# Kernel optimization log

Hardware: AMD Instinct MI355X
Metric: run time of the kernel (lower is better)

The kernel has to match this reference:

```python
import jax, jax.numpy as jnp
import numpy as np

NUM_SELECTS = 2
NOISE_EPS = 0.01
LOSS_COEF = 0.01
INV_SQRT2 = 0.7071067811865476


def _phi(z):
    # standard normal CDF
    return 0.5 * (1.0 + jax.lax.erf(z * INV_SQRT2))


def _cv_squared(v, eps=1e-10):
    # torch .var() uses unbiased estimator (ddof=1)
    return jnp.var(v, ddof=1) / (jnp.mean(v) ** 2 + eps)


def setup_inputs() -> dict:
    key = jax.random.key(0)
    ks = jax.random.split(key, 5)
    T, D, E = 8192, 4096, 16
    return {
        "x": jax.random.normal(ks[0], (T, D), jnp.float32),
        "gate_w1": jax.random.normal(ks[1], (E, D), jnp.float32) * 0.02,
        "gate_w2": jax.random.normal(ks[2], (E, E), jnp.float32) * 0.02,
        "noise_w": jax.random.normal(ks[3], (E, D), jnp.float32) * 0.02,
        "noise": jax.random.normal(ks[4], (T, E), jnp.float32),
    }


def reference(x, gate_w1, gate_w2, noise_w, noise):
    T = x.shape[0]
    # gate network: Linear -> tanh -> Linear (no biases)
    logits_gate = jnp.tanh(x @ gate_w1.T) @ gate_w2.T          # [T, E]
    noise_control = jax.nn.softplus(x @ noise_w.T) + NOISE_EPS  # [T, E]
    logits_noise = noise * noise_control                        # [T, E]
    logits = logits_gate + logits_noise

    # top (k+1) for load-balancing thresholds
    top_logits, top_indices = jax.lax.top_k(logits, NUM_SELECTS + 1)
    top_k_logits = top_logits[:, :NUM_SELECTS]
    top_k_indices = top_indices[:, :NUM_SELECTS]
    top_k_scores = jax.nn.softmax(top_k_logits, axis=1)

    # importance: scatter top-k scores back to [T, E]
    rows = jnp.arange(T)[:, None]
    scores_filtered = jnp.zeros_like(logits).at[rows, top_k_indices].set(top_k_scores)
    importance = scores_filtered.sum(0)  # [E]

    # load: prob each expert would be in the top-k under the noise model
    thr_in = top_logits[:, NUM_SELECTS][:, None]        # (k+1)-th largest
    thr_out = top_logits[:, NUM_SELECTS - 1][:, None]   # k-th largest
    is_in = logits_noise > thr_in
    prob_if_in = _phi((logits_gate - thr_in) / noise_control)
    prob_if_out = _phi((logits_gate - thr_out) / noise_control)
    load = jnp.where(is_in, prob_if_in, prob_if_out).sum(0)  # [E]

    gate_loss = (_cv_squared(importance) + _cv_squared(load)) * LOSS_COEF
    return top_k_indices, top_k_scores, gate_loss
```

## Files before the change

### kernel.cpp

```cpp
#include <hip/hip_runtime.h>
#include <math.h>

#define TT 8192
#define DD 4096

typedef float  f32x4  __attribute__((ext_vector_type(4)));
typedef short  bf16x8 __attribute__((ext_vector_type(8)));
typedef unsigned int u32;

typedef __attribute__((address_space(3))) void        lds_vp;
typedef const __attribute__((address_space(1))) void  gbl_vp;
#define GLD(gp_, lp_) __builtin_amdgcn_global_load_lds((gbl_vp*)(gp_), (lds_vp*)(lp_), 16, 0, 0)

__global__ __launch_bounds__(128)
void split_w(const float* __restrict__ gw1, const float* __restrict__ nw,
             u32* __restrict__ wfrag) {
  const int s = blockIdx.x;
  const int t = threadIdx.x;
  const int h = t >> 6, l = t & 63;
  const int e = h * 16 + (l & 15);
  const float* src = ((e < 16) ? (gw1 + (size_t)e * DD) : (nw + (size_t)(e - 16) * DD))
                     + s * 32 + ((l >> 4) << 3);
  float f[8];
  *(float4*)&f[0] = *(const float4*)src;
  *(float4*)&f[4] = *(const float4*)(src + 4);
  u32 u0[8], u1[8], u2[8];
#pragma unroll
  for (int i = 0; i < 8; ++i) {
    u0[i] = __float_as_uint(f[i]);
    const float r1 = f[i] - __uint_as_float(u0[i] & 0xFFFF0000u);
    u1[i] = __float_as_uint(r1);
    const float r2 = r1 - __uint_as_float(u1[i] & 0xFFFF0000u);
    u2[i] = __float_as_uint(r2);
  }
  const size_t base = ((size_t)s * 2 + h) * 256 + l * 4;
#define PK(U) make_uint4((U[0]>>16)|(U[1]&0xFFFF0000u), (U[2]>>16)|(U[3]&0xFFFF0000u), \
                         (U[4]>>16)|(U[5]&0xFFFF0000u), (U[6]>>16)|(U[7]&0xFFFF0000u))
  *(uint4*)(wfrag + base)                 = PK(u0);
  *(uint4*)(wfrag + base + 128 * 512)     = PK(u1);
  *(uint4*)(wfrag + base + 2 * 128 * 512) = PK(u2);
#undef PK
}

__global__ __launch_bounds__(1024, 4)
void gate_mega(const float* __restrict__ x, const u32* __restrict__ wfrag,
               const float* __restrict__ noise, const float* __restrict__ gw2,
               float* __restrict__ out, float* __restrict__ part2) {
  __shared__ __align__(16) u32 ldsb[2][8][6][256];
  __shared__ float red[8][1024];
  __shared__ float sg2[256];
  const int t = threadIdx.x;
  const int v = t >> 6, l = t & 63;
  const int w = v & 7;
  const int m = v >> 3;
  const int rt = blockIdx.x;
  if (t < 256) sg2[t] = gw2[t];

  const int r = l & 15, c = l >> 4;
  const float* xp = x + (size_t)(rt * 32 + m * 16 + r) * DD + w * 512 + (c << 3);

  const u32* srcb[3];
  u32* dst0[3];
  u32* dst1[3];
#pragma unroll
  for (int i = 0; i < 3; ++i) {
    const int q = 3 * v + i, s = q / 6, p = q % 6;
    srcb[i] = wfrag + (size_t)(p >> 1) * 65536 + (p & 1) * 256
                    + (size_t)s * 16 * 512 + (l << 2);
    dst0[i] = &ldsb[0][s][p][0];
    dst1[i] = &ldsb[1][s][p][0];
  }

#pragma unroll
  for (int i = 0; i < 3; ++i) GLD(srcb[i], dst0[i]);
  asm volatile("s_waitcnt vmcnt(0)" ::: "memory");
  asm volatile("s_barrier" ::: "memory");

  f32x4 ag0 = {0,0,0,0}, ag1 = ag0, ag2 = ag0, an0 = ag0, an1 = ag0, an2 = ag0;

#pragma unroll 2
  for (int sl = 0; sl < 16; ++sl) {
    if (sl + 1 < 16) {
#pragma unroll
      for (int i = 0; i < 3; ++i)
        GLD(srcb[i] + (size_t)(sl + 1) * 512, (sl & 1) ? dst0[i] : dst1[i]);
    }

    const u32* wb = &ldsb[sl & 1][w][0][0] + (l << 2);
    const bf16x8 bg0 = *(const bf16x8*)(wb);
    const bf16x8 bn0 = *(const bf16x8*)(wb + 256);
    const bf16x8 bg1 = *(const bf16x8*)(wb + 512);
    const bf16x8 bn1 = *(const bf16x8*)(wb + 768);
    const bf16x8 bg2 = *(const bf16x8*)(wb + 1024);
    const bf16x8 bn2 = *(const bf16x8*)(wb + 1280);

    float f[8];
    *(float4*)&f[0] = *(const float4*)(xp + sl * 32);
    *(float4*)&f[4] = *(const float4*)(xp + sl * 32 + 4);

    u32 pk[12] __attribute__((aligned(16)));
#pragma unroll
    for (int p = 0; p < 4; ++p) {
      const float fa = f[2 * p], fb = f[2 * p + 1];
      const u32  a  = __float_as_uint(fa);
      const float ra1 = fa - __uint_as_float(a & 0xFFFF0000u);
      const u32  a1 = __float_as_uint(ra1);
      const float ra2 = ra1 - __uint_as_float(a1 & 0xFFFF0000u);
      const u32  a2 = __float_as_uint(ra2);
      const u32  b  = __float_as_uint(fb);
      const float rb1 = fb - __uint_as_float(b & 0xFFFF0000u);
      const u32  b1 = __float_as_uint(rb1);
      const float rb2 = rb1 - __uint_as_float(b1 & 0xFFFF0000u);
      const u32  b2 = __float_as_uint(rb2);
      pk[p]     = (a  >> 16) | (b  & 0xFFFF0000u);
      pk[4 + p] = (a1 >> 16) | (b1 & 0xFFFF0000u);
      pk[8 + p] = (a2 >> 16) | (b2 & 0xFFFF0000u);
    }
    const bf16x8 a0 = *(const bf16x8*)&pk[0];
    const bf16x8 a1 = *(const bf16x8*)&pk[4];
    const bf16x8 a2 = *(const bf16x8*)&pk[8];

    ag0 = __builtin_amdgcn_mfma_f32_16x16x32_bf16(a0, bg0, ag0, 0, 0, 0);
    an0 = __builtin_amdgcn_mfma_f32_16x16x32_bf16(a0, bn0, an0, 0, 0, 0);
    ag1 = __builtin_amdgcn_mfma_f32_16x16x32_bf16(a0, bg1, ag1, 0, 0, 0);
    an1 = __builtin_amdgcn_mfma_f32_16x16x32_bf16(a0, bn1, an1, 0, 0, 0);
    ag2 = __builtin_amdgcn_mfma_f32_16x16x32_bf16(a1, bg0, ag2, 0, 0, 0);
    an2 = __builtin_amdgcn_mfma_f32_16x16x32_bf16(a1, bn0, an2, 0, 0, 0);
    ag0 = __builtin_amdgcn_mfma_f32_16x16x32_bf16(a0, bg2, ag0, 0, 0, 0);
    an0 = __builtin_amdgcn_mfma_f32_16x16x32_bf16(a0, bn2, an0, 0, 0, 0);
    ag1 = __builtin_amdgcn_mfma_f32_16x16x32_bf16(a1, bg1, ag1, 0, 0, 0);
    an1 = __builtin_amdgcn_mfma_f32_16x16x32_bf16(a1, bn1, an1, 0, 0, 0);
    ag2 = __builtin_amdgcn_mfma_f32_16x16x32_bf16(a2, bg0, ag2, 0, 0, 0);
    an2 = __builtin_amdgcn_mfma_f32_16x16x32_bf16(a2, bn0, an2, 0, 0, 0);

    asm volatile("s_waitcnt vmcnt(0)" ::: "memory");
    asm volatile("s_barrier" ::: "memory");
  }

  const f32x4 cg = ag0 + ag1 + ag2;
  const f32x4 cn = an0 + an1 + an2;
#pragma unroll
  for (int j = 0; j < 4; ++j) {
    red[w][m * 512 + r * 16 + (c * 4 + j)]        = cg[j];
    red[w][m * 512 + (16 + r) * 16 + (c * 4 + j)] = cn[j];
  }
  __syncthreads();
  {
    float s = red[0][t];
#pragma unroll
    for (int ww = 1; ww < 8; ++ww) s += red[ww][t];
    red[0][t] = s;
  }
  __syncthreads();

  if (t < 32) {
    const int mg = t >> 4, rr = t & 15;
    const int row = rt * 32 + t;
    float dot[32];
#pragma unroll
    for (int e = 0; e < 32; ++e) dot[e] = red[0][mg * 512 + e * 16 + rr];
    float h[16];
#pragma unroll
    for (int e = 0; e < 16; ++e) h[e] = tanhf(dot[e]);
    float lg[16], nc[16], ln[16], lo[16];
#pragma unroll
    for (int j = 0; j < 16; ++j) {
      float s = 0.f;
#pragma unroll
      for (int e = 0; e < 16; ++e) s = fmaf(h[e], sg2[j * 16 + e], s);
      lg[j] = s;
      const float vv = dot[16 + j];
      nc[j] = fmaxf(vv, 0.f) + log1pf(expf(-fabsf(vv))) + 0.01f;
      ln[j] = noise[(size_t)row * 16 + j] * nc[j];
      lo[j] = lg[j] + ln[j];
    }
    int i0 = 0; float m0 = lo[0];
#pragma unroll
    for (int j = 1; j < 16; ++j) if (lo[j] > m0) { m0 = lo[j]; i0 = j; }
    int i1 = -1; float m1 = -1e30f;
#pragma unroll
    for (int j = 0; j < 16; ++j) if (j != i0 && lo[j] > m1) { m1 = lo[j]; i1 = j; }
    float m2 = -1e30f;
#pragma unroll
    for (int j = 0; j < 16; ++j) if (j != i0 && j != i1 && lo[j] > m2) m2 = lo[j];

    const float e1 = expf(m1 - m0);
    const float s0 = 1.f / (1.f + e1);
    const float s1 = e1 / (1.f + e1);
    out[(size_t)row * 2]             = (float)i0;
    out[(size_t)row * 2 + 1]         = (float)i1;
    out[16384 + (size_t)row * 2]     = s0;
    out[16384 + (size_t)row * 2 + 1] = s1;

    float cacc[32];
#pragma unroll
    for (int j = 0; j < 16; ++j) {
      cacc[j] = (j == i0) ? s0 : ((j == i1) ? s1 : 0.f);
      const bool in = ln[j] > m2;
      const float thr = in ? m2 : m1;
      const float z = (lg[j] - thr) / nc[j];
      cacc[16 + j] = 0.5f * (1.f + erff(z * 0.70710678118654752f));
    }
#pragma unroll
    for (int off = 1; off < 16; off <<= 1) {
#pragma unroll
      for (int k = 0; k < 32; ++k) cacc[k] += __shfl_xor(cacc[k], off, 16);
    }
    const int g = rt * 2 + mg;
    float v0 = 0.f, v1 = 0.f;
#pragma unroll
    for (int k = 0; k < 16; ++k) if (rr == k) { v0 = cacc[k]; v1 = cacc[16 + k]; }
    part2[(size_t)g * 32 + rr]      = v0;
    part2[(size_t)g * 32 + 16 + rr] = v1;
  }
}

__global__ __launch_bounds__(256)
void gate_loss_k(const float* __restrict__ part2, float* __restrict__ out) {
  __shared__ float sred[8][32];
  const int t = threadIdx.x;
  const int k = t & 31, s = t >> 5;
  float acc = 0.f;
#pragma unroll 8
  for (int i = 0; i < 64; ++i) acc += part2[(size_t)(s * 64 + i) * 32 + k];
  sred[s][k] = acc;
  __syncthreads();
  if (t == 0) {
    float res = 0.f;
    for (int g = 0; g < 2; ++g) {
      float vals[16];
      float mu = 0.f;
      for (int j = 0; j < 16; ++j) {
        float s2 = 0.f;
        for (int ss = 0; ss < 8; ++ss) s2 += sred[ss][g * 16 + j];
        vals[j] = s2;
        mu += s2;
      }
      mu *= (1.f / 16.f);
      float var = 0.f;
      for (int j = 0; j < 16; ++j) { const float d = vals[j] - mu; var += d * d; }
      var *= (1.f / 15.f);
      res += var / (mu * mu + 1e-10f);
    }
    out[32768] = res * 0.01f;
  }
}

extern "C" void kernel_launch(void* const* d_in, const int* in_sizes, int n_in,
                              void* d_out, int out_size, void* d_ws, size_t ws_size,
                              hipStream_t stream) {
  const float* x     = (const float*)d_in[0];
  const float* gw1   = (const float*)d_in[1];
  const float* gw2   = (const float*)d_in[2];
  const float* nw    = (const float*)d_in[3];
  const float* noise = (const float*)d_in[4];
  float* out   = (float*)d_out;
  u32*   wfrag = (u32*)d_ws;
  float* part2 = (float*)((char*)d_ws + (size_t)768 * 1024);
  split_w<<<128, 128, 0, stream>>>(gw1, nw, wfrag);
  gate_mega<<<256, 1024, 0, stream>>>(x, wfrag, noise, gw2, out, part2);
  gate_loss_k<<<1, 256, 0, stream>>>(part2, out);
}
```

Measured before the change: 61.21 us.

## Load weight fragments directly from global memory instead of LDS double-buffering

Removes the LDS double buffer and the global_load_lds staging of split weight fragments, so each wave reads its bf16 weight fragments straight from global memory (L2-resident) in the k-loop. This drops the per-iteration waitcnt and barrier and frees LDS, and the launch-bounds occupancy hint rises from 4 to 8 with a larger unroll. In exchange, each wave issues more global loads, since the fragments are no longer shared across the two row-halves, and latency hiding now depends on unrolling and occupancy.

```diff
diff --git a/kernel.cpp b/kernel.cpp
--- a/kernel.cpp
+++ b/kernel.cpp
@@ -7,10 +7,6 @@
 typedef float  f32x4  __attribute__((ext_vector_type(4)));
 typedef short  bf16x8 __attribute__((ext_vector_type(8)));
 typedef unsigned int u32;
-
-typedef __attribute__((address_space(3))) void        lds_vp;
-typedef const __attribute__((address_space(1))) void  gbl_vp;
-#define GLD(gp_, lp_) __builtin_amdgcn_global_load_lds((gbl_vp*)(gp_), (lds_vp*)(lp_), 16, 0, 0)
 
 __global__ __launch_bounds__(128)
 void split_w(const float* __restrict__ gw1, const float* __restrict__ nw,
@@ -42,11 +38,10 @@
 #undef PK
 }
 
-__global__ __launch_bounds__(1024, 4)
+__global__ __launch_bounds__(1024, 8)
 void gate_mega(const float* __restrict__ x, const u32* __restrict__ wfrag,
                const float* __restrict__ noise, const float* __restrict__ gw2,
                float* __restrict__ out, float* __restrict__ part2) {
-  __shared__ __align__(16) u32 ldsb[2][8][6][256];
   __shared__ float red[8][1024];
   __shared__ float sg2[256];
   const int t = threadIdx.x;
@@ -58,45 +53,23 @@
 
   const int r = l & 15, c = l >> 4;
   const float* xp = x + (size_t)(rt * 32 + m * 16 + r) * DD + w * 512 + (c << 3);
-
-  const u32* srcb[3];
-  u32* dst0[3];
-  u32* dst1[3];
-#pragma unroll
-  for (int i = 0; i < 3; ++i) {
-    const int q = 3 * v + i, s = q / 6, p = q % 6;
-    srcb[i] = wfrag + (size_t)(p >> 1) * 65536 + (p & 1) * 256
-                    + (size_t)s * 16 * 512 + (l << 2);
-    dst0[i] = &ldsb[0][s][p][0];
-    dst1[i] = &ldsb[1][s][p][0];
-  }
-
-#pragma unroll
-  for (int i = 0; i < 3; ++i) GLD(srcb[i], dst0[i]);
-  asm volatile("s_waitcnt vmcnt(0)" ::: "memory");
-  asm volatile("s_barrier" ::: "memory");
+  const u32* wfl = wfrag + (size_t)l * 4 + (size_t)(w * 16) * 512;
 
   f32x4 ag0 = {0,0,0,0}, ag1 = ag0, ag2 = ag0, an0 = ag0, an1 = ag0, an2 = ag0;
 
-#pragma unroll 2
+#pragma unroll 4
   for (int sl = 0; sl < 16; ++sl) {
-    if (sl + 1 < 16) {
-#pragma unroll
-      for (int i = 0; i < 3; ++i)
-        GLD(srcb[i] + (size_t)(sl + 1) * 512, (sl & 1) ? dst0[i] : dst1[i]);
-    }
-
-    const u32* wb = &ldsb[sl & 1][w][0][0] + (l << 2);
-    const bf16x8 bg0 = *(const bf16x8*)(wb);
-    const bf16x8 bn0 = *(const bf16x8*)(wb + 256);
-    const bf16x8 bg1 = *(const bf16x8*)(wb + 512);
-    const bf16x8 bn1 = *(const bf16x8*)(wb + 768);
-    const bf16x8 bg2 = *(const bf16x8*)(wb + 1024);
-    const bf16x8 bn2 = *(const bf16x8*)(wb + 1280);
-
     float f[8];
     *(float4*)&f[0] = *(const float4*)(xp + sl * 32);
     *(float4*)&f[4] = *(const float4*)(xp + sl * 32 + 4);
+
+    const u32* wb = wfl + (size_t)sl * 512;
+    const bf16x8 bg0 = *(const bf16x8*)(wb);
+    const bf16x8 bn0 = *(const bf16x8*)(wb + 256);
+    const bf16x8 bg1 = *(const bf16x8*)(wb + 128 * 512);
+    const bf16x8 bn1 = *(const bf16x8*)(wb + 128 * 512 + 256);
+    const bf16x8 bg2 = *(const bf16x8*)(wb + 2 * 128 * 512);
+    const bf16x8 bn2 = *(const bf16x8*)(wb + 2 * 128 * 512 + 256);
 
     u32 pk[12] __attribute__((aligned(16)));
 #pragma unroll
@@ -132,9 +105,6 @@
     an1 = __builtin_amdgcn_mfma_f32_16x16x32_bf16(a1, bn1, an1, 0, 0, 0);
     ag2 = __builtin_amdgcn_mfma_f32_16x16x32_bf16(a2, bg0, ag2, 0, 0, 0);
     an2 = __builtin_amdgcn_mfma_f32_16x16x32_bf16(a2, bn0, an2, 0, 0, 0);
-
-    asm volatile("s_waitcnt vmcnt(0)" ::: "memory");
-    asm volatile("s_barrier" ::: "memory");
   }
 
   const f32x4 cg = ag0 + ag1 + ag2;
```

Measured after the change: 102.5 us. 67.4% more time.

## Triple-buffer weight LDS staging with prefetch distance two and partial waitcnt

Applied to the files above, without the earlier changes.

Replaces the double-buffered weight staging with a three-slot ring in LDS, prefetching two slices ahead. Each iteration now waits only until the older slice has landed (vmcnt(3)) and needs a single barrier before compute, instead of a full drain plus barrier after compute. The gw2 matrix is loaded via async LDS load, and the reduction scratch aliases the weight buffers to keep LDS use in check. The launch-bounds occupancy hint is dropped. The vmcnt(3) wait also counts the x global loads, so whether the wait still guarantees the slice has arrived depends on how the compiler orders those loads.

```diff
diff --git a/kernel.cpp b/kernel.cpp
--- a/kernel.cpp
+++ b/kernel.cpp
@@ -42,51 +42,56 @@
 #undef PK
 }
 
-__global__ __launch_bounds__(1024, 4)
+__global__ __launch_bounds__(1024)
 void gate_mega(const float* __restrict__ x, const u32* __restrict__ wfrag,
                const float* __restrict__ noise, const float* __restrict__ gw2,
                float* __restrict__ out, float* __restrict__ part2) {
-  __shared__ __align__(16) u32 ldsb[2][8][6][256];
-  __shared__ float red[8][1024];
+  __shared__ __align__(16) u32 bufB[3][8][6][256];
   __shared__ float sg2[256];
+  float* red = (float*)&bufB[1][0][0][0];
+
   const int t = threadIdx.x;
   const int v = t >> 6, l = t & 63;
   const int w = v & 7;
   const int m = v >> 3;
   const int rt = blockIdx.x;
-  if (t < 256) sg2[t] = gw2[t];
 
   const int r = l & 15, c = l >> 4;
   const float* xp = x + (size_t)(rt * 32 + m * 16 + r) * DD + w * 512 + (c << 3);
 
   const u32* srcb[3];
-  u32* dst0[3];
-  u32* dst1[3];
+  int dsto[3];
 #pragma unroll
   for (int i = 0; i < 3; ++i) {
     const int q = 3 * v + i, s = q / 6, p = q % 6;
     srcb[i] = wfrag + (size_t)(p >> 1) * 65536 + (p & 1) * 256
                     + (size_t)s * 16 * 512 + (l << 2);
-    dst0[i] = &ldsb[0][s][p][0];
-    dst1[i] = &ldsb[1][s][p][0];
-  }
-
-#pragma unroll
-  for (int i = 0; i < 3; ++i) GLD(srcb[i], dst0[i]);
-  asm volatile("s_waitcnt vmcnt(0)" ::: "memory");
-  asm volatile("s_barrier" ::: "memory");
+    dsto[i] = (s * 6 + p) * 256;
+  }
+  u32* const b0 = &bufB[0][0][0][0];
+  u32* const b1 = &bufB[1][0][0][0];
+  u32* const b2 = &bufB[2][0][0][0];
+
+  if (v == 0) GLD(gw2 + (l << 2), &sg2[0]);
+#pragma unroll
+  for (int i = 0; i < 3; ++i) GLD(srcb[i], b0 + dsto[i]);
+#pragma unroll
+  for (int i = 0; i < 3; ++i) GLD(srcb[i] + 512, b1 + dsto[i]);
 
   f32x4 ag0 = {0,0,0,0}, ag1 = ag0, ag2 = ag0, an0 = ag0, an1 = ag0, an2 = ag0;
 
-#pragma unroll 2
   for (int sl = 0; sl < 16; ++sl) {
-    if (sl + 1 < 16) {
-#pragma unroll
-      for (int i = 0; i < 3; ++i)
-        GLD(srcb[i] + (size_t)(sl + 1) * 512, (sl & 1) ? dst0[i] : dst1[i]);
-    }
-
-    const u32* wb = &ldsb[sl & 1][w][0][0] + (l << 2);
+    if (sl < 15) asm volatile("s_waitcnt vmcnt(3)" ::: "memory");
+    else         asm volatile("s_waitcnt vmcnt(0)" ::: "memory");
+    __builtin_amdgcn_s_barrier();
+
+    if (sl + 2 < 16) {
+      u32* const bn = (((sl + 2) % 3) == 0) ? b0 : ((((sl + 2) % 3) == 1) ? b1 : b2);
+#pragma unroll
+      for (int i = 0; i < 3; ++i) GLD(srcb[i] + (size_t)(sl + 2) * 512, bn + dsto[i]);
+    }
+
+    const u32* wb = &bufB[sl % 3][w][0][0] + (l << 2);
     const bf16x8 bg0 = *(const bf16x8*)(wb);
     const bf16x8 bn0 = *(const bf16x8*)(wb + 256);
     const bf16x8 bg1 = *(const bf16x8*)(wb + 512);
@@ -132,24 +137,23 @@
     an1 = __builtin_amdgcn_mfma_f32_16x16x32_bf16(a1, bn1, an1, 0, 0, 0);
     ag2 = __builtin_amdgcn_mfma_f32_16x16x32_bf16(a2, bg0, ag2, 0, 0, 0);
     an2 = __builtin_amdgcn_mfma_f32_16x16x32_bf16(a2, bn0, an2, 0, 0, 0);
-
-    asm volatile("s_waitcnt vmcnt(0)" ::: "memory");
-    asm volatile("s_barrier" ::: "memory");
-  }
+  }
+
+  __syncthreads();
 
   const f32x4 cg = ag0 + ag1 + ag2;
   const f32x4 cn = an0 + an1 + an2;
 #pragma unroll
   for (int j = 0; j < 4; ++j) {
-    red[w][m * 512 + r * 16 + (c * 4 + j)]        = cg[j];
-    red[w][m * 512 + (16 + r) * 16 + (c * 4 + j)] = cn[j];
+    red[w * 1024 + m * 512 + r * 16 + (c * 4 + j)]        = cg[j];
+    red[w * 1024 + m * 512 + (16 + r) * 16 + (c * 4 + j)] = cn[j];
   }
   __syncthreads();
   {
-    float s = red[0][t];
-#pragma unroll
-    for (int ww = 1; ww < 8; ++ww) s += red[ww][t];
-    red[0][t] = s;
+    float s = red[t];
+#pragma unroll
+    for (int ww = 1; ww < 8; ++ww) s += red[ww * 1024 + t];
+    red[t] = s;
   }
   __syncthreads();
 
@@ -158,7 +162,7 @@
     const int row = rt * 32 + t;
     float dot[32];
 #pragma unroll
-    for (int e = 0; e < 32; ++e) dot[e] = red[0][mg * 512 + e * 16 + rr];
+    for (int e = 0; e < 32; ++e) dot[e] = red[mg * 512 + e * 16 + rr];
     float h[16];
 #pragma unroll
     for (int e = 0; e < 16; ++e) h[e] = tanhf(dot[e]);
```

New measurement: 60.59 us. About the same (-1.0%).
